# Kernel optimization log

Hardware: AMD Instinct MI355X
Metric: run time of the kernel (lower is better)

Reference implementation:

```python
import jax, jax.numpy as jnp
import numpy as np

N = 4096
D = 1024  # hidden_size == att_size


def setup_inputs() -> dict:
    key = jax.random.key(0)
    ks = jax.random.split(key, 10)
    s = 0.02
    return {
        "q": jax.random.normal(ks[0], (N, D), jnp.float32),
        "k": jax.random.normal(ks[1], (N, D), jnp.float32),
        "v": jax.random.normal(ks[2], (N, D), jnp.float32),
        "bias": jax.random.normal(ks[3], (N, N), jnp.float32) * s,
        "Wq": jax.random.normal(ks[4], (D, D), jnp.float32) * s,
        "bq": jnp.zeros((D,), jnp.float32),
        "Wk": jax.random.normal(ks[5], (D, D), jnp.float32) * s,
        "bk": jnp.zeros((D,), jnp.float32),
        "Wv": jax.random.normal(ks[6], (D, D), jnp.float32) * s,
        "bv": jnp.zeros((D,), jnp.float32),
    }


def reference(q, k, v, bias, Wq, bq, Wk, bk, Wv, bv):
    d = q.shape[-1]
    scale = d ** (-0.5)
    # QKV projections (nn.Linear: x @ W.T + b)
    qp = (q @ Wq.T + bq) * scale          # [N, D]
    kp = k @ Wk.T + bk                    # [N, D]
    vp = v @ Wv.T + bv                    # [N, D]
    # full N x N attention (single head, pseudo-batch of 1 in the original)
    scores = qp @ kp.T                    # [N, N]
    att = jax.nn.softmax(scores, axis=-1) + bias  # POST-softmax bias add
    # dropout is identity in eval mode; original casts weights to fp32 here
    out = att.astype(jnp.float32) @ vp    # [N, D]
    return out
```

## Files before the change

### kernel.cpp

```cpp
#include <hip/hip_runtime.h>
#include <hip/hip_bf16.h>
#include <stdint.h>

typedef unsigned short u16;
using bf16x8 = __attribute__((ext_vector_type(8))) __bf16;
using f32x4  = __attribute__((ext_vector_type(4))) float;

__device__ __forceinline__ u16 f2bf(float f) {
    union { float f; unsigned u; } a; a.f = f;
    unsigned u = a.u;
    u += 0x7fffu + ((u >> 16) & 1u);
    return (u16)(u >> 16);
}
__device__ __forceinline__ float bf2f(unsigned bits_hi16) {
    union { unsigned u; float f; } a; a.u = bits_hi16; return a.f;
}

__device__ __forceinline__ void gload_lds16(const void* g, void* l) {
    __builtin_amdgcn_global_load_lds(
        (const __attribute__((address_space(1))) void*)g,
        (__attribute__((address_space(3))) void*)l, 16, 0, 0);
}

__device__ __forceinline__ void xcd_swz(int nx, int ny, int& x, int& y, int& z) {
    const int flat = (int)blockIdx.x + nx * ((int)blockIdx.y + ny * (int)blockIdx.z);
    const int cpx = (nx * ny * (int)gridDim.z) >> 3;
    const int s = (flat & 7) * cpx + (flat >> 3);
    x = s % nx;
    const int t = s / nx;
    y = t % ny;
    z = t / ny;
}

__device__ __forceinline__ void gemm_core(const u16* __restrict__ A,
                                          const u16* __restrict__ B,
                                          int lda, int ldb, int kLen,
                                          int bm, int bn,
                                          u16* sA, u16* sB,
                                          f32x4 acc[4][4])
{
    const int tid  = threadIdx.x;
    const int lane = tid & 63;
    const int wm   = (tid >> 7) & 1;
    const int wn   = (tid >> 6) & 1;

    const u16* Ag0 = A + (long)(bm * 128 + (tid >> 2)) * lda + (tid & 3) * 8;
    const u16* Ag1 = Ag0 + (long)64 * lda;
    const u16* Bg0 = B + (long)(bn * 128 + (tid >> 2)) * ldb + (tid & 3) * 8;
    const u16* Bg1 = Bg0 + (long)64 * ldb;
    u16* la = sA + tid * 8;
    u16* lb = sB + tid * 8;

    const int rfo  = (wm * 64 + (lane & 15)) * 32 + (lane >> 4) * 8;
    const int rfoB = (wn * 64 + (lane & 15)) * 32 + (lane >> 4) * 8;

    for (int k0 = 0; k0 < kLen; k0 += 64) {
        gload_lds16(Ag0 + k0, la);
        gload_lds16(Ag1 + k0, la + 2048);
        gload_lds16(Bg0 + k0, lb);
        gload_lds16(Bg1 + k0, lb + 2048);
        gload_lds16(Ag0 + k0 + 32, la + 4096);
        gload_lds16(Ag1 + k0 + 32, la + 6144);
        gload_lds16(Bg0 + k0 + 32, lb + 4096);
        gload_lds16(Bg1 + k0 + 32, lb + 6144);
        __syncthreads();
#pragma unroll
        for (int h = 0; h < 2; h++) {
            const u16* ra = sA + h * 4096 + rfo;
            const u16* rb = sB + h * 4096 + rfoB;
            bf16x8 af[4], bfr[4];
#pragma unroll
            for (int i = 0; i < 4; i++) af[i]  = *(const bf16x8*)(ra + i * 512);
#pragma unroll
            for (int i = 0; i < 4; i++) bfr[i] = *(const bf16x8*)(rb + i * 512);
#pragma unroll
            for (int mi = 0; mi < 4; mi++)
#pragma unroll
                for (int ni = 0; ni < 4; ni++)
                    acc[mi][ni] = __builtin_amdgcn_mfma_f32_16x16x32_bf16(
                        af[mi], bfr[ni], acc[mi][ni], 0, 0, 0);
        }
        __syncthreads();
    }
}

__device__ __forceinline__ void gemm256_core(const u16* __restrict__ A,
                                             const u16* __restrict__ B,
                                             int lda, int ldb, int T,
                                             int rowA0, int rowB0,
                                             u16* lds,
                                             f32x4 acc[8][4],
                                             int wm, int wn)
{
    const int tid = (int)threadIdx.x;
    const int l = tid & 63;
    const int w = tid >> 6;

    const int srcswz = 8 * ((l & 3) ^ ((l >> 3) & 3));
    const u16* pA = A + (long)(rowA0 + w * 32 + (l >> 2)) * lda + srcswz;
    const u16* pB = B + (long)(rowB0 + w * 32 + (l >> 2)) * ldb + srcswz;
    const int dstbase = w * 1024 + l * 8;

    const int fsw = 8 * ((l >> 4) ^ ((l >> 1) & 3));
    const int fA = (wm * 128 + (l & 15)) * 32 + fsw;
    const int fB = (wn * 64  + (l & 15)) * 32 + fsw;

    bf16x8 af0[8], bf0[4], af1[8], bf1[4];

#define STAGE(tile, kh)                                                        \
    {                                                                          \
        const long co = (long)(tile) * 64 + (kh) * 32;                         \
        u16* d = lds + (((tile) & 1) << 15) + ((kh) << 13) + dstbase;          \
        gload_lds16(pA + co, d);                                               \
        gload_lds16(pA + co + 16 * (long)lda, d + 512);                        \
        gload_lds16(pB + co, d + 16384);                                       \
        gload_lds16(pB + co + 16 * (long)ldb, d + 16384 + 512);                \
    }

#define RD(af, bfr, tile, ks)                                                  \
    {                                                                          \
        const u16* Ar = lds + (((tile) & 1) << 15) + ((ks) << 13);             \
        const u16* Br = Ar + 16384;                                            \
        _Pragma("unroll")                                                      \
        for (int mi = 0; mi < 8; mi++)                                         \
            af[mi] = *(const bf16x8*)(Ar + fA + mi * 512);                     \
        _Pragma("unroll")                                                      \
        for (int ni = 0; ni < 4; ni++)                                         \
            bfr[ni] = *(const bf16x8*)(Br + fB + ni * 512);                    \
    }

#define MF(af, bfr, lo)                                                        \
    {                                                                          \
        __builtin_amdgcn_s_setprio(1);                                         \
        _Pragma("unroll")                                                      \
        for (int mi = (lo); mi < (lo) + 4; mi++)                               \
            _Pragma("unroll")                                                  \
            for (int ni = 0; ni < 4; ni++)                                     \
                acc[mi][ni] = __builtin_amdgcn_mfma_f32_16x16x32_bf16(         \
                    af[mi], bfr[ni], acc[mi][ni], 0, 0, 0);                    \
        __builtin_amdgcn_s_setprio(0);                                         \
    }

    STAGE(0, 0); STAGE(0, 1); STAGE(1, 0); STAGE(1, 1);
    asm volatile("s_waitcnt vmcnt(8)" ::: "memory");
    __builtin_amdgcn_s_barrier();
    RD(af0, bf0, 0, 0);
    asm volatile("s_waitcnt lgkmcnt(0)" ::: "memory");
    __builtin_amdgcn_s_barrier();

    for (int t = 0; t < T; ++t) {
        const int t2  = (t + 2 < T) ? t + 2 : T - 1;
        const int t1c = (t + 1 < T) ? t + 1 : T - 1;

        RD(af1, bf1, t, 1);
        MF(af0, bf0, 0);

        STAGE(t2, 0);
        MF(af0, bf0, 4);
        asm volatile("s_waitcnt lgkmcnt(0)" ::: "memory");
        __builtin_amdgcn_s_barrier();

        asm volatile("s_waitcnt vmcnt(4)" ::: "memory");
        RD(af0, bf0, t1c, 0);
        MF(af1, bf1, 0);

        STAGE(t2, 1);
        MF(af1, bf1, 4);
        asm volatile("s_waitcnt lgkmcnt(0)" ::: "memory");
        __builtin_amdgcn_s_barrier();
    }
    asm volatile("s_waitcnt vmcnt(0)" ::: "memory");

#undef STAGE
#undef RD
#undef MF
}

__global__ __launch_bounds__(256)
void cast6(const float* __restrict__ q, const float* __restrict__ k,
           const float* __restrict__ v, const float* __restrict__ wq,
           const float* __restrict__ wk, const float* __restrict__ wv,
           u16* __restrict__ qb, u16* __restrict__ kb, u16* __restrict__ vb,
           u16* __restrict__ wqb, u16* __restrict__ wkb, u16* __restrict__ wvb,
           int nqkv, int nw)
{
    const int z = blockIdx.y;
    const float* s; u16* d; int n;
    switch (z) {
        case 0:  s = q;  d = qb;  n = nqkv; break;
        case 1:  s = k;  d = kb;  n = nqkv; break;
        case 2:  s = v;  d = vb;  n = nqkv; break;
        case 3:  s = wq; d = wqb; n = nw;   break;
        case 4:  s = wk; d = wkb; n = nw;   break;
        default: s = wv; d = wvb; n = nw;   break;
    }
    long i = ((long)blockIdx.x * 256 + threadIdx.x) * 8;
    if (i >= n) return;
    float4 a = *(const float4*)(s + i);
    float4 b = *(const float4*)(s + i + 4);
    ushort4 o0, o1;
    o0.x = f2bf(a.x); o0.y = f2bf(a.y); o0.z = f2bf(a.z); o0.w = f2bf(a.w);
    o1.x = f2bf(b.x); o1.y = f2bf(b.y); o1.z = f2bf(b.z); o1.w = f2bf(b.w);
    *(ushort4*)(d + i)     = o0;
    *(ushort4*)(d + i + 4) = o1;
}

__global__ __launch_bounds__(256, 2)
void proj_gemm(const u16* __restrict__ qb, const u16* __restrict__ kb,
               const u16* __restrict__ vb, const u16* __restrict__ wqb,
               const u16* __restrict__ wkb, const u16* __restrict__ wvb,
               const float* __restrict__ bq, const float* __restrict__ bk,
               const float* __restrict__ bv,
               u16* __restrict__ qp, u16* __restrict__ kp, u16* __restrict__ vpT)
{
    __shared__ __align__(16) u16 sA[8192];
    __shared__ __align__(16) u16 sB[8192];
    int bx, by, bz;
    xcd_swz(8, 32, bx, by, bz);
    const int z = bz;
    const u16* A = (z == 0) ? qb : (z == 1) ? kb : vb;
    const u16* B = (z == 0) ? wqb : (z == 1) ? wkb : wvb;
    const float* bias = (z == 0) ? bq : (z == 1) ? bk : bv;
    u16* OUT = (z == 0) ? qp : (z == 1) ? kp : vpT;
    const float scale = (z == 0) ? 0.03125f : 1.0f;

    f32x4 acc[4][4] = {};
    gemm_core(A, B, 1024, 1024, 1024, by, bx, sA, sB, acc);

    const int lane = threadIdx.x & 63;
    const int wm   = (threadIdx.x >> 7) & 1;
    const int wn   = (threadIdx.x >> 6) & 1;
    const int m0 = by * 128 + wm * 64 + ((lane >> 4) << 2);
    const int n0 = bx * 128 + wn * 64 + (lane & 15);
#pragma unroll
    for (int mi = 0; mi < 4; mi++)
#pragma unroll
        for (int ni = 0; ni < 4; ni++) {
            const int gm = m0 + mi * 16;
            const int gn = n0 + ni * 16;
            const float bb = bias[gn];
#pragma unroll
            for (int r = 0; r < 4; r++) {
                float val = (acc[mi][ni][r] + bb) * scale;
                if (z < 2) OUT[(long)(gm + r) * 1024 + gn] = f2bf(val);
                else       OUT[(long)gn * 4096 + gm + r]   = f2bf(val);
            }
        }
}

__global__ __launch_bounds__(256, 2)
void vproj_gemm(const u16* __restrict__ wvb, const u16* __restrict__ vb,
                const float* __restrict__ bv, u16* __restrict__ vpT)
{
    __shared__ __align__(16) u16 sA[8192];
    __shared__ __align__(16) u16 sB[8192];
    f32x4 acc[4][4] = {};
    gemm_core(wvb, vb, 1024, 1024, 1024, blockIdx.y, blockIdx.x, sA, sB, acc);

    const int lane = threadIdx.x & 63;
    const int wm   = (threadIdx.x >> 7) & 1;
    const int wn   = (threadIdx.x >> 6) & 1;
    const int m0 = blockIdx.y * 128 + wm * 64 + ((lane >> 4) << 2);
    const int n0 = blockIdx.x * 128 + wn * 64 + (lane & 15);
#pragma unroll
    for (int mi = 0; mi < 4; mi++)
#pragma unroll
        for (int ni = 0; ni < 4; ni++) {
            const int gm = m0 + mi * 16;
            const int gn = n0 + ni * 16;
#pragma unroll
            for (int r = 0; r < 4; r++)
                vpT[(long)(gm + r) * 4096 + gn] = f2bf(acc[mi][ni][r] + bv[gm + r]);
        }
}

__global__ __launch_bounds__(512, 2)
void score_gemm256(const u16* __restrict__ qp, const u16* __restrict__ kp,
                   u16* __restrict__ S)
{
    __shared__ __align__(16) u16 lds[65536];

    const int flat = (int)blockIdx.x + ((int)blockIdx.y << 4);
    const int sfl = (flat & 7) * 32 + (flat >> 3);
    const int bx = sfl & 15;
    const int by = sfl >> 4;

    const int l  = (int)threadIdx.x & 63;
    const int w  = (int)threadIdx.x >> 6;
    const int wm = w >> 2;
    const int wn = w & 3;

    f32x4 acc[8][4] = {};
    gemm256_core(qp, kp, 1024, 1024, 16, by * 256, bx * 256, lds, acc, wm, wn);

    const int gm0 = by * 256 + wm * 128 + ((l >> 4) << 2);
    const int gn0 = bx * 256 + wn * 64 + (l & 15);
#pragma unroll
    for (int mi = 0; mi < 8; mi++)
#pragma unroll
        for (int ni = 0; ni < 4; ni++) {
            const int gm = gm0 + mi * 16;
            const int gn = gn0 + ni * 16;
#pragma unroll
            for (int r = 0; r < 4; r++)
                S[(long)(gm + r) * 4096 + gn] = f2bf(acc[mi][ni][r]);
        }
}

__global__ __launch_bounds__(256)
void softmax_bias(const u16* __restrict__ S, const float* __restrict__ bias,
                  u16* __restrict__ att)
{
    const long row = blockIdx.x;
    const int tid = threadIdx.x;
    const u16* srow = S + row * 4096 + tid * 16;

    float v[16];
    {
        uint4 a = *(const uint4*)(srow);
        uint4 b = *(const uint4*)(srow + 8);
        unsigned w[8] = {a.x, a.y, a.z, a.w, b.x, b.y, b.z, b.w};
#pragma unroll
        for (int i = 0; i < 8; i++) {
            v[2 * i]     = bf2f(w[i] << 16);
            v[2 * i + 1] = bf2f(w[i] & 0xffff0000u);
        }
    }
    float mx = v[0];
#pragma unroll
    for (int i = 1; i < 16; i++) mx = fmaxf(mx, v[i]);
#pragma unroll
    for (int o = 32; o >= 1; o >>= 1) mx = fmaxf(mx, __shfl_xor(mx, o, 64));
    __shared__ float red[8];
    if ((tid & 63) == 0) red[tid >> 6] = mx;
    __syncthreads();
    mx = fmaxf(fmaxf(red[0], red[1]), fmaxf(red[2], red[3]));
    float sum = 0.f;
#pragma unroll
    for (int i = 0; i < 16; i++) { v[i] = __expf(v[i] - mx); sum += v[i]; }
#pragma unroll
    for (int o = 32; o >= 1; o >>= 1) sum += __shfl_xor(sum, o, 64);
    if ((tid & 63) == 0) red[4 + (tid >> 6)] = sum;
    __syncthreads();
    const float inv = 1.0f / (red[4] + red[5] + red[6] + red[7]);

    const float4* brow = (const float4*)(bias + row * 4096 + tid * 16);
    unsigned o[8];
#pragma unroll
    for (int i = 0; i < 4; i++) {
        float4 b = brow[i];
        unsigned lo = f2bf(v[4 * i + 0] * inv + b.x);
        unsigned hi = f2bf(v[4 * i + 1] * inv + b.y);
        o[2 * i] = lo | (hi << 16);
        lo = f2bf(v[4 * i + 2] * inv + b.z);
        hi = f2bf(v[4 * i + 3] * inv + b.w);
        o[2 * i + 1] = lo | (hi << 16);
    }
    u16* arow = att + row * 4096 + tid * 16;
    *(uint4*)(arow)     = make_uint4(o[0], o[1], o[2], o[3]);
    *(uint4*)(arow + 8) = make_uint4(o[4], o[5], o[6], o[7]);
}

__global__ __launch_bounds__(512, 2)
void out_gemm256(const u16* __restrict__ att, const u16* __restrict__ vpT,
                 float* __restrict__ P)
{
    __shared__ __align__(16) u16 lds[65536];

    int bx, by, bz;
    xcd_swz(4, 16, bx, by, bz);
    const u16* A = att + bz * 1024;
    const u16* B = vpT + bz * 1024;
    float* O = P + (long)bz * 4096 * 1024;

    const int l  = (int)threadIdx.x & 63;
    const int w  = (int)threadIdx.x >> 6;
    const int wm = w >> 2;
    const int wn = w & 3;

    f32x4 acc[8][4] = {};
    gemm256_core(A, B, 4096, 4096, 16, by * 256, bx * 256, lds, acc, wm, wn);

    const int gm0 = by * 256 + wm * 128 + ((l >> 4) << 2);
    const int gn0 = bx * 256 + wn * 64 + (l & 15);
#pragma unroll
    for (int mi = 0; mi < 8; mi++)
#pragma unroll
        for (int ni = 0; ni < 4; ni++) {
            const int gm = gm0 + mi * 16;
            const int gn = gn0 + ni * 16;
#pragma unroll
            for (int r = 0; r < 4; r++)
                O[(long)(gm + r) * 1024 + gn] = acc[mi][ni][r];
        }
}

__global__ __launch_bounds__(256)
void addp4(const float* __restrict__ P, float* __restrict__ O)
{
    long i = ((long)blockIdx.x * 256 + threadIdx.x) * 4;
    const long st = 4194304;
    float4 a = *(const float4*)(P + i);
    float4 b = *(const float4*)(P + st + i);
    float4 c = *(const float4*)(P + 2 * st + i);
    float4 d = *(const float4*)(P + 3 * st + i);
    float4 r;
    r.x = (a.x + b.x) + (c.x + d.x);
    r.y = (a.y + b.y) + (c.y + d.y);
    r.z = (a.z + b.z) + (c.z + d.z);
    r.w = (a.w + b.w) + (c.w + d.w);
    *(float4*)(O + i) = r;
}

extern "C" void kernel_launch(void* const* d_in, const int* in_sizes, int n_in,
                              void* d_out, int out_size, void* d_ws, size_t ws_size,
                              hipStream_t stream)
{
    const float* q    = (const float*)d_in[0];
    const float* k    = (const float*)d_in[1];
    const float* v    = (const float*)d_in[2];
    const float* bias = (const float*)d_in[3];
    const float* Wq   = (const float*)d_in[4];
    const float* bq   = (const float*)d_in[5];
    const float* Wk   = (const float*)d_in[6];
    const float* bk   = (const float*)d_in[7];
    const float* Wv   = (const float*)d_in[8];
    const float* bv   = (const float*)d_in[9];
    float* out = (float*)d_out;

    uint8_t* ws = (uint8_t*)d_ws;
    const size_t MB = 1u << 20;
    u16* qb  = (u16*)(ws);
    u16* kb  = (u16*)(ws + 8 * MB);
    u16* vb  = (u16*)(ws + 16 * MB);
    u16* wqb = (u16*)(ws + 24 * MB);
    u16* wkb = (u16*)(ws + 26 * MB);
    u16* wvb = (u16*)(ws + 28 * MB);
    u16* qp  = (u16*)(ws + 30 * MB);
    u16* kp  = (u16*)(ws + 38 * MB);
    u16* vpT = (u16*)(ws + 46 * MB);
    u16* S   = (u16*)(ws + 54 * MB);
    u16* att = (u16*)(ws);
    float* P = (float*)(ws + 54 * MB);

    cast6<<<dim3(2048, 6), 256, 0, stream>>>(q, k, v, Wq, Wk, Wv,
                                             qb, kb, vb, wqb, wkb, wvb,
                                             4096 * 1024, 1024 * 1024);
    proj_gemm<<<dim3(8, 32, 2), 256, 0, stream>>>(qb, kb, vb, wqb, wkb, wvb,
                                                  bq, bk, bv, qp, kp, vpT);
    vproj_gemm<<<dim3(32, 8), 256, 0, stream>>>(wvb, vb, bv, vpT);
    score_gemm256<<<dim3(16, 16), 512, 0, stream>>>(qp, kp, S);
    softmax_bias<<<dim3(4096), 256, 0, stream>>>(S, bias, att);
    out_gemm256<<<dim3(4, 16, 4), 512, 0, stream>>>(att, vpT, P);
    addp4<<<dim3(4096), 256, 0, stream>>>(P, out);
}
```

Before: 302.7 us.

## Restructure 256-tile GEMM main loop into four-phase half-tile pipeline

Replaces the two-stage register double-buffered loop (full 8x4 A fragments, prefetch two tiles ahead) with a four-phase schedule per K tile. Each phase loads half of the A fragments, issues split A/B global-to-LDS stages for the next tile, and runs 16 MFMAs between barriers. The aim is to cut register pressure and interleave LDS reads, global loads and MFMAs more finely. The trade-off is more barriers per iteration and only one tile of lookahead, which could expose memory latency.

```diff
diff --git a/kernel.cpp b/kernel.cpp
--- a/kernel.cpp
+++ b/kernel.cpp
@@ -92,88 +92,110 @@
                                              f32x4 acc[8][4],
                                              int wm, int wn)
 {
-    const int tid = (int)threadIdx.x;
-    const int l = tid & 63;
-    const int w = tid >> 6;
+    const int l = (int)threadIdx.x & 63;
+    const int w = (int)threadIdx.x >> 6;
 
     const int srcswz = 8 * ((l & 3) ^ ((l >> 3) & 3));
     const u16* pA = A + (long)(rowA0 + w * 32 + (l >> 2)) * lda + srcswz;
     const u16* pB = B + (long)(rowB0 + w * 32 + (l >> 2)) * ldb + srcswz;
-    const int dstbase = w * 1024 + l * 8;
+    const int dstb = w * 1024 + l * 8;
 
     const int fsw = 8 * ((l >> 4) ^ ((l >> 1) & 3));
     const int fA = (wm * 128 + (l & 15)) * 32 + fsw;
     const int fB = (wn * 64  + (l & 15)) * 32 + fsw;
 
-    bf16x8 af0[8], bf0[4], af1[8], bf1[4];
-
-#define STAGE(tile, kh)                                                        \
-    {                                                                          \
-        const long co = (long)(tile) * 64 + (kh) * 32;                         \
-        u16* d = lds + (((tile) & 1) << 15) + ((kh) << 13) + dstbase;          \
-        gload_lds16(pA + co, d);                                               \
-        gload_lds16(pA + co + 16 * (long)lda, d + 512);                        \
-        gload_lds16(pB + co, d + 16384);                                       \
-        gload_lds16(pB + co + 16 * (long)ldb, d + 16384 + 512);                \
-    }
-
-#define RD(af, bfr, tile, ks)                                                  \
-    {                                                                          \
-        const u16* Ar = lds + (((tile) & 1) << 15) + ((ks) << 13);             \
-        const u16* Br = Ar + 16384;                                            \
+    bf16x8 alo[4], ahi[4], bk0[4], bk1[4];
+
+#define STG_A(tile, kh)                                                        \
+    {                                                                          \
+        const u16* s = pA + (long)(tile) * 64 + (kh) * 32;                     \
+        u16* d = lds + (((tile) & 1) << 15) + ((kh) << 13) + dstb;             \
+        gload_lds16(s, d);                                                     \
+        gload_lds16(s + 16 * (long)lda, d + 512);                              \
+    }
+#define STG_B(tile, kh)                                                        \
+    {                                                                          \
+        const u16* s = pB + (long)(tile) * 64 + (kh) * 32;                     \
+        u16* d = lds + (((tile) & 1) << 15) + ((kh) << 13) + 16384 + dstb;     \
+        gload_lds16(s, d);                                                     \
+        gload_lds16(s + 16 * (long)ldb, d + 512);                              \
+    }
+#define RD_A(dst, tile, ks, mih)                                               \
+    {                                                                          \
+        const u16* Ar = lds + (((tile) & 1) << 15) + ((ks) << 13) + fA +       \
+                        (mih) * 2048;                                          \
         _Pragma("unroll")                                                      \
-        for (int mi = 0; mi < 8; mi++)                                         \
-            af[mi] = *(const bf16x8*)(Ar + fA + mi * 512);                     \
+        for (int i = 0; i < 4; i++) dst[i] = *(const bf16x8*)(Ar + i * 512);   \
+    }
+#define RD_B(dst, tile, ks)                                                    \
+    {                                                                          \
+        const u16* Br = lds + (((tile) & 1) << 15) + ((ks) << 13) + 16384 + fB;\
         _Pragma("unroll")                                                      \
-        for (int ni = 0; ni < 4; ni++)                                         \
-            bfr[ni] = *(const bf16x8*)(Br + fB + ni * 512);                    \
-    }
-
-#define MF(af, bfr, lo)                                                        \
+        for (int i = 0; i < 4; i++) dst[i] = *(const bf16x8*)(Br + i * 512);   \
+    }
+#define MF16(a_, b_, lo)                                                       \
     {                                                                          \
         __builtin_amdgcn_s_setprio(1);                                         \
         _Pragma("unroll")                                                      \
-        for (int mi = (lo); mi < (lo) + 4; mi++)                               \
+        for (int mi = 0; mi < 4; mi++)                                         \
             _Pragma("unroll")                                                  \
             for (int ni = 0; ni < 4; ni++)                                     \
-                acc[mi][ni] = __builtin_amdgcn_mfma_f32_16x16x32_bf16(         \
-                    af[mi], bfr[ni], acc[mi][ni], 0, 0, 0);                    \
+                acc[(lo) + mi][ni] = __builtin_amdgcn_mfma_f32_16x16x32_bf16(  \
+                    a_[mi], b_[ni], acc[(lo) + mi][ni], 0, 0, 0);              \
         __builtin_amdgcn_s_setprio(0);                                         \
     }
-
-    STAGE(0, 0); STAGE(0, 1); STAGE(1, 0); STAGE(1, 1);
-    asm volatile("s_waitcnt vmcnt(8)" ::: "memory");
-    __builtin_amdgcn_s_barrier();
-    RD(af0, bf0, 0, 0);
-    asm volatile("s_waitcnt lgkmcnt(0)" ::: "memory");
-    __builtin_amdgcn_s_barrier();
+#define BAR()  __builtin_amdgcn_s_barrier()
+#define LGKM0()                                                                \
+    {                                                                          \
+        asm volatile("s_waitcnt lgkmcnt(0)" ::: "memory");                     \
+        __builtin_amdgcn_sched_barrier(0);                                     \
+    }
+#define VM4() asm volatile("s_waitcnt vmcnt(4)" ::: "memory")
+
+    STG_A(0, 0); STG_B(0, 0);
+    STG_A(0, 1); STG_B(0, 1);
+    VM4();
+    BAR();
 
     for (int t = 0; t < T; ++t) {
-        const int t2  = (t + 2 < T) ? t + 2 : T - 1;
-        const int t1c = (t + 1 < T) ? t + 1 : T - 1;
-
-        RD(af1, bf1, t, 1);
-        MF(af0, bf0, 0);
-
-        STAGE(t2, 0);
-        MF(af0, bf0, 4);
-        asm volatile("s_waitcnt lgkmcnt(0)" ::: "memory");
-        __builtin_amdgcn_s_barrier();
-
-        asm volatile("s_waitcnt vmcnt(4)" ::: "memory");
-        RD(af0, bf0, t1c, 0);
-        MF(af1, bf1, 0);
-
-        STAGE(t2, 1);
-        MF(af1, bf1, 4);
-        asm volatile("s_waitcnt lgkmcnt(0)" ::: "memory");
-        __builtin_amdgcn_s_barrier();
+        const int ts = (t + 1 < T) ? t + 1 : T - 1;
+
+        RD_A(alo, t, 0, 0); RD_B(bk0, t, 0);
+        STG_A(ts, 0);
+        BAR(); LGKM0();
+        MF16(alo, bk0, 0);
+        BAR();
+
+        RD_A(ahi, t, 0, 1);
+        STG_B(ts, 0);
+        VM4();
+        BAR(); LGKM0();
+        MF16(ahi, bk0, 4);
+        BAR();
+
+        RD_A(alo, t, 1, 0); RD_B(bk1, t, 1);
+        STG_A(ts, 1);
+        BAR(); LGKM0();
+        MF16(alo, bk1, 0);
+        BAR();
+
+        RD_A(ahi, t, 1, 1);
+        STG_B(ts, 1);
+        VM4();
+        BAR(); LGKM0();
+        MF16(ahi, bk1, 4);
+        BAR();
     }
     asm volatile("s_waitcnt vmcnt(0)" ::: "memory");
 
-#undef STAGE
-#undef RD
-#undef MF
+#undef STG_A
+#undef STG_B
+#undef RD_A
+#undef RD_B
+#undef MF16
+#undef BAR
+#undef LGKM0
+#undef VM4
 }
 
 __global__ __launch_bounds__(256)
```

New measurement: 302.7 us. No clear change (+0.0%).

## Use 32x32x16 MFMA in 256-tile GEMM core and merge V projection launch

Applied to the files above, without the earlier changes.

Switches the shared 256x256 GEMM core used by the score and output GEMMs from 16x16x32 to 32x32x16 bf16 MFMA. The LDS fragment reads and the epilogue row mapping are reworked to match the 32x32 accumulator layout. Separately, the V projection is folded into proj_gemm as a third z slice so one launch replaces two. The larger MFMA shape means fewer instructions and fewer LDS fragment reads per FLOP, at the cost of a different swizzle pattern that may add bank conflicts, and the epilogue stores become more scattered.

```diff
diff --git a/kernel.cpp b/kernel.cpp
--- a/kernel.cpp
+++ b/kernel.cpp
@@ -5,6 +5,7 @@
 typedef unsigned short u16;
 using bf16x8 = __attribute__((ext_vector_type(8))) __bf16;
 using f32x4  = __attribute__((ext_vector_type(4))) float;
+using f32x16 = __attribute__((ext_vector_type(16))) float;
 
 __device__ __forceinline__ u16 f2bf(float f) {
     union { float f; unsigned u; } a; a.f = f;
@@ -89,91 +90,106 @@
                                              int lda, int ldb, int T,
                                              int rowA0, int rowB0,
                                              u16* lds,
-                                             f32x4 acc[8][4],
+                                             f32x16 acc[4][2],
                                              int wm, int wn)
 {
-    const int tid = (int)threadIdx.x;
-    const int l = tid & 63;
-    const int w = tid >> 6;
+    const int l = (int)threadIdx.x & 63;
+    const int w = (int)threadIdx.x >> 6;
 
     const int srcswz = 8 * ((l & 3) ^ ((l >> 3) & 3));
     const u16* pA = A + (long)(rowA0 + w * 32 + (l >> 2)) * lda + srcswz;
     const u16* pB = B + (long)(rowB0 + w * 32 + (l >> 2)) * ldb + srcswz;
-    const int dstbase = w * 1024 + l * 8;
-
-    const int fsw = 8 * ((l >> 4) ^ ((l >> 1) & 3));
-    const int fA = (wm * 128 + (l & 15)) * 32 + fsw;
-    const int fB = (wn * 64  + (l & 15)) * 32 + fsw;
-
-    bf16x8 af0[8], bf0[4], af1[8], bf1[4];
-
-#define STAGE(tile, kh)                                                        \
+    const int dstb = w * 1024 + l * 8;
+
+    const int swz = (l >> 1) & 3;
+    const int hi  = l >> 5;
+    const int s0  = 8 * (hi ^ swz);
+    const int s1  = 8 * ((2 + hi) ^ swz);
+    const int RA  = (wm * 128 + (l & 31)) * 32;
+    const int RB  = (wn * 64  + (l & 31)) * 32;
+
+    bf16x8 af0[4][2], bf0[2][2], af1[4][2], bf1[2][2];
+
+#define STG(tile, kh)                                                          \
     {                                                                          \
         const long co = (long)(tile) * 64 + (kh) * 32;                         \
-        u16* d = lds + (((tile) & 1) << 15) + ((kh) << 13) + dstbase;          \
+        u16* d = lds + (((tile) & 1) << 15) + ((kh) << 13) + dstb;             \
         gload_lds16(pA + co, d);                                               \
         gload_lds16(pA + co + 16 * (long)lda, d + 512);                        \
         gload_lds16(pB + co, d + 16384);                                       \
         gload_lds16(pB + co + 16 * (long)ldb, d + 16384 + 512);                \
     }
 
-#define RD(af, bfr, tile, ks)                                                  \
+#define RD_SET(af, bfr, tile, ksh)                                             \
     {                                                                          \
-        const u16* Ar = lds + (((tile) & 1) << 15) + ((ks) << 13);             \
-        const u16* Br = Ar + 16384;                                            \
+        const u16* base = lds + (((tile) & 1) << 15) + ((ksh) << 13);          \
         _Pragma("unroll")                                                      \
-        for (int mi = 0; mi < 8; mi++)                                         \
-            af[mi] = *(const bf16x8*)(Ar + fA + mi * 512);                     \
+        for (int mi = 0; mi < 4; mi++) {                                       \
+            af[mi][0] = *(const bf16x8*)(base + RA + mi * 1024 + s0);          \
+            af[mi][1] = *(const bf16x8*)(base + RA + mi * 1024 + s1);          \
+        }                                                                      \
         _Pragma("unroll")                                                      \
-        for (int ni = 0; ni < 4; ni++)                                         \
-            bfr[ni] = *(const bf16x8*)(Br + fB + ni * 512);                    \
-    }
-
-#define MF(af, bfr, lo)                                                        \
+        for (int ni = 0; ni < 2; ni++) {                                       \
+            bfr[ni][0] = *(const bf16x8*)(base + 16384 + RB + ni * 1024 + s0); \
+            bfr[ni][1] = *(const bf16x8*)(base + 16384 + RB + ni * 1024 + s1); \
+        }                                                                      \
+    }
+
+#define MF8(a_, b_, milo)                                                      \
     {                                                                          \
         __builtin_amdgcn_s_setprio(1);                                         \
         _Pragma("unroll")                                                      \
-        for (int mi = (lo); mi < (lo) + 4; mi++)                               \
+        for (int mi = (milo); mi < (milo) + 2; mi++)                           \
             _Pragma("unroll")                                                  \
-            for (int ni = 0; ni < 4; ni++)                                     \
-                acc[mi][ni] = __builtin_amdgcn_mfma_f32_16x16x32_bf16(         \
-                    af[mi], bfr[ni], acc[mi][ni], 0, 0, 0);                    \
+            for (int ni = 0; ni < 2; ni++)                                     \
+                _Pragma("unroll")                                              \
+                for (int kb = 0; kb < 2; kb++)                                 \
+                    acc[mi][ni] = __builtin_amdgcn_mfma_f32_32x32x16_bf16(     \
+                        a_[mi][kb], b_[ni][kb], acc[mi][ni], 0, 0, 0);         \
         __builtin_amdgcn_s_setprio(0);                                         \
     }
-
-    STAGE(0, 0); STAGE(0, 1); STAGE(1, 0); STAGE(1, 1);
+#define BAR()  __builtin_amdgcn_s_barrier()
+#define LGKM0()                                                                \
+    {                                                                          \
+        asm volatile("s_waitcnt lgkmcnt(0)" ::: "memory");                     \
+        __builtin_amdgcn_sched_barrier(0);                                     \
+    }
+
+    STG(0, 0); STG(0, 1); STG(1, 0); STG(1, 1);
     asm volatile("s_waitcnt vmcnt(8)" ::: "memory");
-    __builtin_amdgcn_s_barrier();
-    RD(af0, bf0, 0, 0);
-    asm volatile("s_waitcnt lgkmcnt(0)" ::: "memory");
-    __builtin_amdgcn_s_barrier();
+    BAR();
+    RD_SET(af0, bf0, 0, 0);
+    LGKM0();
+    BAR();
 
     for (int t = 0; t < T; ++t) {
-        const int t2  = (t + 2 < T) ? t + 2 : T - 1;
+        const int ts  = (t + 2 < T) ? t + 2 : T - 1;
         const int t1c = (t + 1 < T) ? t + 1 : T - 1;
 
-        RD(af1, bf1, t, 1);
-        MF(af0, bf0, 0);
-
-        STAGE(t2, 0);
-        MF(af0, bf0, 4);
-        asm volatile("s_waitcnt lgkmcnt(0)" ::: "memory");
-        __builtin_amdgcn_s_barrier();
-
+        RD_SET(af1, bf1, t, 1);
+        MF8(af0, bf0, 0);
+
+        STG(ts, 0);
+        MF8(af0, bf0, 2);
+        LGKM0();
         asm volatile("s_waitcnt vmcnt(4)" ::: "memory");
-        RD(af0, bf0, t1c, 0);
-        MF(af1, bf1, 0);
-
-        STAGE(t2, 1);
-        MF(af1, bf1, 4);
-        asm volatile("s_waitcnt lgkmcnt(0)" ::: "memory");
-        __builtin_amdgcn_s_barrier();
+        BAR();
+
+        RD_SET(af0, bf0, t1c, 0);
+        MF8(af1, bf1, 0);
+
+        STG(ts, 1);
+        MF8(af1, bf1, 2);
+        LGKM0();
+        BAR();
     }
     asm volatile("s_waitcnt vmcnt(0)" ::: "memory");
 
-#undef STAGE
-#undef RD
-#undef MF
+#undef STG
+#undef RD_SET
+#undef MF8
+#undef BAR
+#undef LGKM0
 }
 
 __global__ __launch_bounds__(256)
@@ -218,18 +234,37 @@
     int bx, by, bz;
     xcd_swz(8, 32, bx, by, bz);
     const int z = bz;
-    const u16* A = (z == 0) ? qb : (z == 1) ? kb : vb;
-    const u16* B = (z == 0) ? wqb : (z == 1) ? wkb : wvb;
-    const float* bias = (z == 0) ? bq : (z == 1) ? bk : bv;
-    u16* OUT = (z == 0) ? qp : (z == 1) ? kp : vpT;
-    const float scale = (z == 0) ? 0.03125f : 1.0f;
 
     f32x4 acc[4][4] = {};
-    gemm_core(A, B, 1024, 1024, 1024, by, bx, sA, sB, acc);
-
     const int lane = threadIdx.x & 63;
     const int wm   = (threadIdx.x >> 7) & 1;
     const int wn   = (threadIdx.x >> 6) & 1;
+
+    if (z == 2) {
+        gemm_core(wvb, vb, 1024, 1024, 1024, bx, by, sA, sB, acc);
+        const int m0 = bx * 128 + wm * 64 + ((lane >> 4) << 2);
+        const int n0 = by * 128 + wn * 64 + (lane & 15);
+#pragma unroll
+        for (int mi = 0; mi < 4; mi++)
+#pragma unroll
+            for (int ni = 0; ni < 4; ni++) {
+                const int gm = m0 + mi * 16;
+                const int gn = n0 + ni * 16;
+#pragma unroll
+                for (int r = 0; r < 4; r++)
+                    vpT[(long)(gm + r) * 4096 + gn] = f2bf(acc[mi][ni][r] + bv[gm + r]);
+            }
+        return;
+    }
+
+    const u16* A = (z == 0) ? qb : kb;
+    const u16* B = (z == 0) ? wqb : wkb;
+    const float* bias = (z == 0) ? bq : bk;
+    u16* OUT = (z == 0) ? qp : kp;
+    const float scale = (z == 0) ? 0.03125f : 1.0f;
+
+    gemm_core(A, B, 1024, 1024, 1024, by, bx, sA, sB, acc);
+
     const int m0 = by * 128 + wm * 64 + ((lane >> 4) << 2);
     const int n0 = bx * 128 + wn * 64 + (lane & 15);
 #pragma unroll
@@ -240,37 +275,8 @@
             const int gn = n0 + ni * 16;
             const float bb = bias[gn];
 #pragma unroll
-            for (int r = 0; r < 4; r++) {
-                float val = (acc[mi][ni][r] + bb) * scale;
-                if (z < 2) OUT[(long)(gm + r) * 1024 + gn] = f2bf(val);
-                else       OUT[(long)gn * 4096 + gm + r]   = f2bf(val);
-            }
-        }
-}
-
-__global__ __launch_bounds__(256, 2)
-void vproj_gemm(const u16* __restrict__ wvb, const u16* __restrict__ vb,
-                const float* __restrict__ bv, u16* __restrict__ vpT)
-{
-    __shared__ __align__(16) u16 sA[8192];
-    __shared__ __align__(16) u16 sB[8192];
-    f32x4 acc[4][4] = {};
-    gemm_core(wvb, vb, 1024, 1024, 1024, blockIdx.y, blockIdx.x, sA, sB, acc);
-
-    const int lane = threadIdx.x & 63;
-    const int wm   = (threadIdx.x >> 7) & 1;
-    const int wn   = (threadIdx.x >> 6) & 1;
-    const int m0 = blockIdx.y * 128 + wm * 64 + ((lane >> 4) << 2);
-    const int n0 = blockIdx.x * 128 + wn * 64 + (lane & 15);
-#pragma unroll
-    for (int mi = 0; mi < 4; mi++)
-#pragma unroll
-        for (int ni = 0; ni < 4; ni++) {
-            const int gm = m0 + mi * 16;
-            const int gn = n0 + ni * 16;
-#pragma unroll
             for (int r = 0; r < 4; r++)
-                vpT[(long)(gm + r) * 4096 + gn] = f2bf(acc[mi][ni][r] + bv[gm + r]);
+                OUT[(long)(gm + r) * 1024 + gn] = f2bf((acc[mi][ni][r] + bb) * scale);
         }
 }
 
@@ -290,20 +296,23 @@
     const int wm = w >> 2;
     const int wn = w & 3;
 
-    f32x4 acc[8][4] = {};
+    f32x16 acc[4][2] = {};
     gemm256_core(qp, kp, 1024, 1024, 16, by * 256, bx * 256, lds, acc, wm, wn);
 
-    const int gm0 = by * 256 + wm * 128 + ((l >> 4) << 2);
-    const int gn0 = bx * 256 + wn * 64 + (l & 15);
-#pragma unroll
-    for (int mi = 0; mi < 8; mi++)
-#pragma unroll
-        for (int ni = 0; ni < 4; ni++) {
-            const int gm = gm0 + mi * 16;
-            const int gn = gn0 + ni * 16;
-#pragma unroll
-            for (int r = 0; r < 4; r++)
-                S[(long)(gm + r) * 4096 + gn] = f2bf(acc[mi][ni][r]);
+    const int hi = l >> 5;
+    const int gm0 = by * 256 + wm * 128 + 4 * hi;
+    const int gn0 = bx * 256 + wn * 64 + (l & 31);
+#pragma unroll
+    for (int mi = 0; mi < 4; mi++)
+#pragma unroll
+        for (int ni = 0; ni < 2; ni++) {
+            const int gmb = gm0 + mi * 32;
+            const int gn  = gn0 + ni * 32;
+#pragma unroll
+            for (int r = 0; r < 16; r++) {
+                const int row = gmb + (r & 3) + 8 * (r >> 2);
+                S[(long)row * 4096 + gn] = f2bf(acc[mi][ni][r]);
+            }
         }
 }
 
@@ -378,20 +387,23 @@
     const int wm = w >> 2;
     const int wn = w & 3;
 
-    f32x4 acc[8][4] = {};
+    f32x16 acc[4][2] = {};
     gemm256_core(A, B, 4096, 4096, 16, by * 256, bx * 256, lds, acc, wm, wn);
 
-    const int gm0 = by * 256 + wm * 128 + ((l >> 4) << 2);
-    const int gn0 = bx * 256 + wn * 64 + (l & 15);
-#pragma unroll
-    for (int mi = 0; mi < 8; mi++)
-#pragma unroll
-        for (int ni = 0; ni < 4; ni++) {
-            const int gm = gm0 + mi * 16;
-            const int gn = gn0 + ni * 16;
-#pragma unroll
-            for (int r = 0; r < 4; r++)
-                O[(long)(gm + r) * 1024 + gn] = acc[mi][ni][r];
+    const int hi = l >> 5;
+    const int gm0 = by * 256 + wm * 128 + 4 * hi;
+    const int gn0 = bx * 256 + wn * 64 + (l & 31);
+#pragma unroll
+    for (int mi = 0; mi < 4; mi++)
+#pragma unroll
+        for (int ni = 0; ni < 2; ni++) {
+            const int gmb = gm0 + mi * 32;
+            const int gn  = gn0 + ni * 32;
+#pragma unroll
+            for (int r = 0; r < 16; r++) {
+                const int row = gmb + (r & 3) + 8 * (r >> 2);
+                O[(long)row * 1024 + gn] = acc[mi][ni][r];
+            }
         }
 }
 
@@ -446,9 +458,8 @@
     cast6<<<dim3(2048, 6), 256, 0, stream>>>(q, k, v, Wq, Wk, Wv,
                                              qb, kb, vb, wqb, wkb, wvb,
                                              4096 * 1024, 1024 * 1024);
-    proj_gemm<<<dim3(8, 32, 2), 256, 0, stream>>>(qb, kb, vb, wqb, wkb, wvb,
+    proj_gemm<<<dim3(8, 32, 3), 256, 0, stream>>>(qb, kb, vb, wqb, wkb, wvb,
                                                   bq, bk, bv, qp, kp, vpT);
-    vproj_gemm<<<dim3(32, 8), 256, 0, stream>>>(wvb, vb, bv, vpT);
     score_gemm256<<<dim3(16, 16), 512, 0, stream>>>(qp, kp, S);
     softmax_bias<<<dim3(4096), 256, 0, stream>>>(S, bias, att);
     out_gemm256<<<dim3(4, 16, 4), 512, 0, stream>>>(att, vpT, P);
```

After: 296.4 us. -2.1%, faster.
